# Optimization experiments

Measured on AMD Instinct MI355X. Metric: run time of the kernel, lower is better.

Reference implementation:

```python
import jax, jax.numpy as jnp
import numpy as np

EPS = 1.01e-08
BN_EPS = 1e-5

def conv2d(x, w, b, stride, padding):
    y = jax.lax.conv_general_dilated(x, w, window_strides=stride, padding=padding,
                                     dimension_numbers=('NCHW', 'OIHW', 'NCHW'))
    return y + b[None, :, None, None]

def masknorm(x, mask, mask_norm):
    amp = jnp.sqrt(jnp.sum(x * x, axis=1, keepdims=True) + EPS)  # (B,1,F,T)
    if mask is None:
        return x / amp
    if mask_norm:
        mask_sum = jnp.sum(mask, axis=(2, 3), keepdims=True)
        return x * mask / (amp * mask_sum)
    return x * mask / amp

def flow_attention(q, k, v):
    # Flowformer linear attention, single head. q,k,v: (B, L, D)
    q = jax.nn.sigmoid(q)
    k = jax.nn.sigmoid(k)
    L = q.shape[1]
    sink_in = 1.0 / (jnp.einsum('bld,bd->bl', q + EPS, k.sum(1) + EPS))
    src_out = 1.0 / (jnp.einsum('bld,bd->bl', k + EPS, q.sum(1) + EPS))
    cons_sink = jnp.einsum('bld,bd->bl', q + EPS, (k * src_out[..., None]).sum(1) + EPS)
    cons_src = jnp.einsum('bld,bd->bl', k + EPS, (q * sink_in[..., None]).sum(1) + EPS)
    sink_alloc = jax.nn.sigmoid(cons_sink)
    src_comp = jax.nn.softmax(cons_src, axis=-1) * jnp.asarray(L, q.dtype)
    kv = jnp.einsum('bld,blm->bdm', k, v * src_comp[..., None])  # (B,D,D)
    out = jnp.einsum('bld,bdm->blm', q, kv) * sink_in[..., None] * sink_alloc[..., None]
    return out

def setup_inputs() -> dict:
    key = jax.random.key(0)
    ks = jax.random.split(key, 16)
    B, Cin, H, T = 4, 8, 252, 2048
    D = 12  # emb_dims
    inp = {
        'x': jax.random.normal(ks[0], (B, Cin, H, T), jnp.float32),
        'frame': jax.random.uniform(ks[1], (B, 1, 84, T), jnp.float32),
        # CBLR: Conv2d(8,16,5x5,same) + BatchNorm2d(16) + LeakyReLU
        'w_pre': jax.random.normal(ks[2], (16, 8, 5, 5), jnp.float32) * 0.05,
        'b_pre': jnp.zeros((16,), jnp.float32),
        'bn_gamma': jnp.ones((16,), jnp.float32),
        'bn_beta': jnp.zeros((16,), jnp.float32),
        'bn_mean': jnp.zeros((16,), jnp.float32),
        'bn_var': jnp.ones((16,), jnp.float32),
        'T': jnp.asarray(2.0, jnp.float32),
        'wq_conv': jax.random.normal(ks[3], (D, 16, 3, 3), jnp.float32) * 0.05,
        'bq_conv': jnp.zeros((D,), jnp.float32),
        'wkv_conv': jax.random.normal(ks[4], (D, 16, 3, 3), jnp.float32) * 0.05,
        'bkv_conv': jnp.zeros((D,), jnp.float32),
        # FlowAttention projections (single head, d_model = emb_dims = 12)
        'fa_wq': jax.random.normal(ks[5], (D, D), jnp.float32) * 0.3,
        'fa_bq': jnp.zeros((D,), jnp.float32),
        'fa_wk': jax.random.normal(ks[6], (D, D), jnp.float32) * 0.3,
        'fa_bk': jnp.zeros((D,), jnp.float32),
        'fa_wv': jax.random.normal(ks[7], (D, D), jnp.float32) * 0.3,
        'fa_bv': jnp.zeros((D,), jnp.float32),
        'fa_wo': jax.random.normal(ks[8], (D, D), jnp.float32) * 0.3,
        'fa_bo': jnp.zeros((D,), jnp.float32),
    }
    return inp

def reference(x, frame, w_pre, b_pre, bn_gamma, bn_beta, bn_mean, bn_var, T,
              wq_conv, bq_conv, wkv_conv, bkv_conv,
              fa_wq, fa_bq, fa_wk, fa_bk, fa_wv, fa_bv, fa_wo, fa_bo):
    # pre_encoding: Conv(same) -> BatchNorm(eval) -> LeakyReLU(0.01)
    h = conv2d(x, w_pre, b_pre, (1, 1), [(2, 2), (2, 2)])
    h = (h - bn_mean[None, :, None, None]) * jax.lax.rsqrt(bn_var + BN_EPS)[None, :, None, None]
    h = h * bn_gamma[None, :, None, None] + bn_beta[None, :, None, None]
    h = jnp.where(h >= 0, h, 0.01 * h)
    # embedding convs: kernel 3x3, stride (3,1), padding (0,1) -> (B,D,84,T)
    KV = conv2d(h, wkv_conv, bkv_conv, (3, 1), [(0, 0), (1, 1)])
    KV = masknorm(KV, frame, True) * T
    Q = conv2d(h, wq_conv, bq_conv, (3, 1), [(0, 0), (1, 1)])
    B, D, Fb, Tt = Q.shape
    # flatten spatial grid to a sequence of length L = F*T
    q = Q.reshape(B, D, Fb * Tt).transpose(0, 2, 1)
    kv = KV.reshape(B, D, Fb * Tt).transpose(0, 2, 1)
    qp = q @ fa_wq + fa_bq
    kp = kv @ fa_wk + fa_bk
    vp = kv @ fa_wv + fa_bv
    o = flow_attention(qp, kp, vp)
    o = o @ fa_wo + fa_bo  # dropout disabled (eval)
    emb = o.transpose(0, 2, 1).reshape(B, D, Fb, Tt)
    return emb
```

## Files before the change

### kernel.cpp

```cpp
#include <hip/hip_runtime.h>
#include <math.h>

#define EPSF 1.01e-08f

namespace {
constexpr int NB = 4;
constexpr int HH = 252, TW = 2048;
constexpr int C1 = 16, DD = 12, FF = 84;
constexpr int LLEN = FF * TW;

constexpr size_t OFF_H   = 0;
constexpr size_t SZ_H    = (size_t)NB * C1 * HH * TW;
constexpr size_t SZ_QKV  = (size_t)NB * LLEN * DD;
constexpr size_t OFF_Q   = OFF_H + SZ_H;
constexpr size_t OFF_K   = OFF_Q + SZ_QKV;
constexpr size_t OFF_V   = OFF_K + SZ_QKV;
constexpr size_t OFF_SI  = OFF_V + SZ_QKV;
constexpr size_t OFF_SA  = OFF_SI + (size_t)NB * LLEN;
constexpr size_t OFF_WP  = OFF_SA + (size_t)NB * LLEN;
constexpr size_t OFF_B1  = OFF_WP + 3200;
constexpr size_t OFF_WQT = OFF_B1 + 16;
constexpr size_t OFF_WKT = OFF_WQT + 1728;
constexpr size_t FTOT    = OFF_WKT + 1728;
constexpr size_t DBYTE   = FTOT * sizeof(float);

constexpr int DO_MSUM = 0;
constexpr int DO_KSUM = 4;
constexpr int DO_QSUM = 52;
constexpr int DO_SKQ  = 100;
constexpr int DO_SQS  = 148;
constexpr int DO_SE   = 196;
constexpr int DO_M    = 200;
constexpr int NDBL    = 776;
}

__device__ __forceinline__ float wsum(float v) {
#pragma unroll
  for (int m = 1; m < 64; m <<= 1) v += __shfl_xor(v, m, 64);
  return v;
}
__device__ __forceinline__ double wsumd(double v) {
#pragma unroll
  for (int m = 1; m < 64; m <<= 1) v += __shfl_xor(v, m, 64);
  return v;
}
__device__ __forceinline__ void atomAddD(double* p, double v) { unsafeAtomicAdd(p, v); }
__device__ __forceinline__ float sigm(float x) { return 1.f / (1.f + expf(-x)); }

__global__ void k_prep(const float* __restrict__ w_pre, const float* __restrict__ b_pre,
                       const float* __restrict__ g, const float* __restrict__ be,
                       const float* __restrict__ mean, const float* __restrict__ var,
                       const float* __restrict__ wq, const float* __restrict__ wkv,
                       float* __restrict__ ws) {
  int tid = blockIdx.x * 256 + threadIdx.x;
  int stride = gridDim.x * 256;
  if (tid < 16) {
    float sc = g[tid] / sqrtf(var[tid] + 1e-5f);
    ws[OFF_B1 + tid] = (b_pre[tid] - mean[tid]) * sc + be[tid];
  }
  for (int idx = tid; idx < 3200; idx += stride) {
    int co = idx & 15, r = idx >> 4;
    int ci = r / 25, p = r % 25;
    float sc = g[co] / sqrtf(var[co] + 1e-5f);
    ws[OFF_WP + idx] = w_pre[(co * 8 + ci) * 25 + p] * sc;
  }
  for (int idx = tid; idx < 1728; idx += stride) {
    int d = idx % 12, r = idx / 12;
    ws[OFF_WQT + idx] = wq[d * 144 + r];
    ws[OFF_WKT + idx] = wkv[d * 144 + r];
  }
}

__global__ __launch_bounds__(256, 4) void k_conv1(const float* __restrict__ x,
                                                  const float* __restrict__ wsc,
                                                  float* __restrict__ h) {
  __shared__ __align__(16) float xs[6][520];

  const int cb = blockIdx.x * 512;
  const int y0 = blockIdx.y * 2;
  const int b = blockIdx.z;

  float acc[16][2][2];
#pragma unroll
  for (int co = 0; co < 16; co++)
#pragma unroll
    for (int r = 0; r < 2; r++)
#pragma unroll
      for (int c = 0; c < 2; c++) acc[co][r][c] = 0.f;

  const int lc = (int)threadIdx.x * 2;

  for (int ci = 0; ci < 8; ci++) {
    __syncthreads();
    const float* xc = x + (size_t)(b * 8 + ci) * HH * TW;
    for (int li = threadIdx.x; li < 6 * 520; li += 256) {
      const int r = li / 520;
      const int c = li - r * 520;
      const int gy = y0 - 2 + r;
      const int gx = cb - 2 + c;
      float v = 0.f;
      if (gy >= 0 && gy < HH && gx >= 0 && gx < TW) v = xc[(size_t)gy * TW + gx];
      xs[r][c] = v;
    }
    __syncthreads();

#pragma unroll
    for (int kh = 0; kh < 5; kh++) {
      float ra[6], rb[6];
#pragma unroll
      for (int u = 0; u < 3; u++) {
        const float2 a = *(const float2*)(&xs[kh][lc + 2 * u]);
        const float2 bv = *(const float2*)(&xs[kh + 1][lc + 2 * u]);
        ra[2 * u] = a.x; ra[2 * u + 1] = a.y;
        rb[2 * u] = bv.x; rb[2 * u + 1] = bv.y;
      }
      const float* wrow = wsc + OFF_WP + (size_t)(ci * 25 + kh * 5) * 16;
#pragma unroll
      for (int kw = 0; kw < 5; kw++) {
        const float4 wA = *(const float4*)(wrow + kw * 16);
        const float4 wB = *(const float4*)(wrow + kw * 16 + 4);
        const float4 wC = *(const float4*)(wrow + kw * 16 + 8);
        const float4 wD = *(const float4*)(wrow + kw * 16 + 12);
        const float wv[16] = {wA.x, wA.y, wA.z, wA.w, wB.x, wB.y, wB.z, wB.w,
                              wC.x, wC.y, wC.z, wC.w, wD.x, wD.y, wD.z, wD.w};
        const float x00 = ra[kw], x01 = ra[kw + 1];
        const float x10 = rb[kw], x11 = rb[kw + 1];
#pragma unroll
        for (int co = 0; co < 16; co++) {
          acc[co][0][0] = fmaf(x00, wv[co], acc[co][0][0]);
          acc[co][0][1] = fmaf(x01, wv[co], acc[co][0][1]);
          acc[co][1][0] = fmaf(x10, wv[co], acc[co][1][0]);
          acc[co][1][1] = fmaf(x11, wv[co], acc[co][1][1]);
        }
      }
    }
  }

#pragma unroll
  for (int co = 0; co < 16; co++) {
    const float bb = wsc[OFF_B1 + co];
#pragma unroll
    for (int r = 0; r < 2; r++) {
      float2 o;
      const float z0 = acc[co][r][0] + bb; o.x = (z0 >= 0.f) ? z0 : 0.01f * z0;
      const float z1 = acc[co][r][1] + bb; o.y = (z1 >= 0.f) ? z1 : 0.01f * z1;
      *(float2*)(h + ((size_t)(b * 16 + co) * HH + (y0 + r)) * TW + cb + lc) = o;
    }
  }
}

__global__ void k_masksum(const float* __restrict__ frame, double* __restrict__ dacc) {
  const int b = blockIdx.y;
  const float* fr = frame + (size_t)b * FF * TW;
  double s = 0.0;
  for (int i = blockIdx.x * 256 + threadIdx.x; i < FF * TW; i += gridDim.x * 256)
    s += (double)fr[i];
  s = wsumd(s);
  __shared__ double sm[4];
  int lane = threadIdx.x & 63, wid = threadIdx.x >> 6;
  if (lane == 0) sm[wid] = s;
  __syncthreads();
  if (threadIdx.x == 0) atomAddD(&dacc[DO_MSUM + b], sm[0] + sm[1] + sm[2] + sm[3]);
}

__global__ __launch_bounds__(256, 3) void k_conv2q(
    const float* __restrict__ h, const float* __restrict__ wsc,
    double* __restrict__ dacc,
    const float* __restrict__ fwq, const float* __restrict__ fbq,
    const float* __restrict__ bqc,
    float* __restrict__ qo) {
  const int c0 = (blockIdx.x * 256 + threadIdx.x) * 4;
  const int f = blockIdx.y;
  const int b = blockIdx.z;
  const bool interior = (c0 >= 4) && (c0 + 8 <= TW);

  float aq[12][4];
#pragma unroll
  for (int d = 0; d < 12; d++) {
    const float bq = bqc[d];
#pragma unroll
    for (int j = 0; j < 4; j++) aq[d][j] = bq;
  }

  for (int c = 0; c < 16; c++) {
    const float* hc = h + ((size_t)(b * 16 + c) * HH + 3 * f) * TW;
#pragma unroll
    for (int kh = 0; kh < 3; kh++) {
      const float* row = hc + (size_t)kh * TW;
      float xr[12];
      if (interior) {
#pragma unroll
        for (int v = 0; v < 3; v++)
          *(float4*)(xr + 4 * v) = *(const float4*)(row + c0 - 4 + 4 * v);
      } else {
#pragma unroll
        for (int j = 0; j < 12; j++) {
          int cc = c0 - 4 + j;
          xr[j] = (cc >= 0 && cc < TW) ? row[cc] : 0.f;
        }
      }
      const float* wp = wsc + OFF_WQT + (size_t)(c * 9 + kh * 3) * 12;
#pragma unroll
      for (int kw = 0; kw < 3; kw++) {
        const float4 w0 = *(const float4*)(wp + kw * 12);
        const float4 w1 = *(const float4*)(wp + kw * 12 + 4);
        const float4 w2 = *(const float4*)(wp + kw * 12 + 8);
        const float wv[12] = {w0.x, w0.y, w0.z, w0.w, w1.x, w1.y, w1.z, w1.w,
                              w2.x, w2.y, w2.z, w2.w};
#pragma unroll
        for (int j = 0; j < 4; j++) {
          const float xv = xr[3 + kw + j];
#pragma unroll
          for (int d = 0; d < 12; d++) aq[d][j] = fmaf(xv, wv[d], aq[d][j]);
        }
      }
    }
  }

  float s1[12][4];
#pragma unroll
  for (int d = 0; d < 12; d++) {
    const float bb = fbq[d];
#pragma unroll
    for (int j = 0; j < 4; j++) s1[d][j] = bb;
  }
#pragma unroll
  for (int e = 0; e < 12; e++) {
    const float4 w0 = *(const float4*)(fwq + e * 12);
    const float4 w1 = *(const float4*)(fwq + e * 12 + 4);
    const float4 w2 = *(const float4*)(fwq + e * 12 + 8);
    const float wv[12] = {w0.x, w0.y, w0.z, w0.w, w1.x, w1.y, w1.z, w1.w,
                          w2.x, w2.y, w2.z, w2.w};
#pragma unroll
    for (int j = 0; j < 4; j++) {
      const float a = aq[e][j];
#pragma unroll
      for (int d = 0; d < 12; d++) s1[d][j] = fmaf(a, wv[d], s1[d][j]);
    }
  }

  float qsumP[12];
#pragma unroll
  for (int d = 0; d < 12; d++) qsumP[d] = 0.f;
  const size_t lbase = (size_t)f * TW + c0;
#pragma unroll
  for (int j = 0; j < 4; j++) {
    const size_t o = ((size_t)b * LLEN + lbase + j) * 12;
#pragma unroll
    for (int d = 0; d < 12; d++) {
      const float qv = sigm(s1[d][j]);
      qsumP[d] += qv;
      qo[o + d] = qv;
    }
  }

  __shared__ float red[4 * 12];
  int lane = threadIdx.x & 63, wid = threadIdx.x >> 6;
#pragma unroll
  for (int d = 0; d < 12; d++) {
    float s = wsum(qsumP[d]);
    if (lane == 0) red[wid * 12 + d] = s;
  }
  __syncthreads();
  if (threadIdx.x < 12) {
    float tot = red[threadIdx.x] + red[12 + threadIdx.x] + red[24 + threadIdx.x] + red[36 + threadIdx.x];
    atomAddD(&dacc[DO_QSUM + b * 12 + threadIdx.x], (double)tot);
  }
}

__global__ __launch_bounds__(256, 3) void k_conv2kv(
    const float* __restrict__ h, const float* __restrict__ frame,
    const float* __restrict__ wsc, double* __restrict__ dacc,
    const float* __restrict__ fwk, const float* __restrict__ fbk,
    const float* __restrict__ fwv, const float* __restrict__ fbv,
    const float* __restrict__ bkvc, const float* __restrict__ Tp,
    float* __restrict__ ko, float* __restrict__ vo) {
  const int c0 = (blockIdx.x * 256 + threadIdx.x) * 4;
  const int f = blockIdx.y;
  const int b = blockIdx.z;
  const bool interior = (c0 >= 4) && (c0 + 8 <= TW);

  float akv[12][4];
#pragma unroll
  for (int d = 0; d < 12; d++) {
    const float bk = bkvc[d];
#pragma unroll
    for (int j = 0; j < 4; j++) akv[d][j] = bk;
  }

  for (int c = 0; c < 16; c++) {
    const float* hc = h + ((size_t)(b * 16 + c) * HH + 3 * f) * TW;
#pragma unroll
    for (int kh = 0; kh < 3; kh++) {
      const float* row = hc + (size_t)kh * TW;
      float xr[12];
      if (interior) {
#pragma unroll
        for (int v = 0; v < 3; v++)
          *(float4*)(xr + 4 * v) = *(const float4*)(row + c0 - 4 + 4 * v);
      } else {
#pragma unroll
        for (int j = 0; j < 12; j++) {
          int cc = c0 - 4 + j;
          xr[j] = (cc >= 0 && cc < TW) ? row[cc] : 0.f;
        }
      }
      const float* wp = wsc + OFF_WKT + (size_t)(c * 9 + kh * 3) * 12;
#pragma unroll
      for (int kw = 0; kw < 3; kw++) {
        const float4 w0 = *(const float4*)(wp + kw * 12);
        const float4 w1 = *(const float4*)(wp + kw * 12 + 4);
        const float4 w2 = *(const float4*)(wp + kw * 12 + 8);
        const float wv[12] = {w0.x, w0.y, w0.z, w0.w, w1.x, w1.y, w1.z, w1.w,
                              w2.x, w2.y, w2.z, w2.w};
#pragma unroll
        for (int j = 0; j < 4; j++) {
          const float xv = xr[3 + kw + j];
#pragma unroll
          for (int d = 0; d < 12; d++) akv[d][j] = fmaf(xv, wv[d], akv[d][j]);
        }
      }
    }
  }

  const float msum = (float)dacc[DO_MSUM + b];
  const float Tv = Tp[0];
  const float4 mk4 = *(const float4*)(frame + ((size_t)b * FF + f) * TW + c0);
  const float mks[4] = {mk4.x, mk4.y, mk4.z, mk4.w};
#pragma unroll
  for (int j = 0; j < 4; j++) {
    float ss = EPSF;
#pragma unroll
    for (int d = 0; d < 12; d++) ss = fmaf(akv[d][j], akv[d][j], ss);
    const float sc = mks[j] * Tv / (sqrtf(ss) * msum);
#pragma unroll
    for (int d = 0; d < 12; d++) akv[d][j] *= sc;
  }

  const size_t lbase = (size_t)f * TW + c0;
  float ksumP[12];
#pragma unroll
  for (int d = 0; d < 12; d++) ksumP[d] = 0.f;

  {
    float s2[12][4];
#pragma unroll
    for (int d = 0; d < 12; d++) {
      const float bb = fbk[d];
#pragma unroll
      for (int j = 0; j < 4; j++) s2[d][j] = bb;
    }
#pragma unroll
    for (int e = 0; e < 12; e++) {
      const float4 w0 = *(const float4*)(fwk + e * 12);
      const float4 w1 = *(const float4*)(fwk + e * 12 + 4);
      const float4 w2 = *(const float4*)(fwk + e * 12 + 8);
      const float wv[12] = {w0.x, w0.y, w0.z, w0.w, w1.x, w1.y, w1.z, w1.w,
                            w2.x, w2.y, w2.z, w2.w};
#pragma unroll
      for (int j = 0; j < 4; j++) {
        const float a = akv[e][j];
#pragma unroll
        for (int d = 0; d < 12; d++) s2[d][j] = fmaf(a, wv[d], s2[d][j]);
      }
    }
#pragma unroll
    for (int j = 0; j < 4; j++) {
      const size_t o = ((size_t)b * LLEN + lbase + j) * 12;
#pragma unroll
      for (int d = 0; d < 12; d++) {
        const float kk = sigm(s2[d][j]);
        ksumP[d] += kk;
        ko[o + d] = kk;
      }
    }
  }

  {
    float s3[12][4];
#pragma unroll
    for (int d = 0; d < 12; d++) {
      const float bb = fbv[d];
#pragma unroll
      for (int j = 0; j < 4; j++) s3[d][j] = bb;
    }
#pragma unroll
    for (int e = 0; e < 12; e++) {
      const float4 w0 = *(const float4*)(fwv + e * 12);
      const float4 w1 = *(const float4*)(fwv + e * 12 + 4);
      const float4 w2 = *(const float4*)(fwv + e * 12 + 8);
      const float wv[12] = {w0.x, w0.y, w0.z, w0.w, w1.x, w1.y, w1.z, w1.w,
                            w2.x, w2.y, w2.z, w2.w};
#pragma unroll
      for (int j = 0; j < 4; j++) {
        const float a = akv[e][j];
#pragma unroll
        for (int d = 0; d < 12; d++) s3[d][j] = fmaf(a, wv[d], s3[d][j]);
      }
    }
#pragma unroll
    for (int j = 0; j < 4; j++) {
      const size_t o = ((size_t)b * LLEN + lbase + j) * 12;
#pragma unroll
      for (int d = 0; d < 12; d++) vo[o + d] = s3[d][j];
    }
  }

  __shared__ float red[4 * 12];
  int lane = threadIdx.x & 63, wid = threadIdx.x >> 6;
#pragma unroll
  for (int d = 0; d < 12; d++) {
    float s = wsum(ksumP[d]);
    if (lane == 0) red[wid * 12 + d] = s;
  }
  __syncthreads();
  if (threadIdx.x < 12) {
    float tot = red[threadIdx.x] + red[12 + threadIdx.x] + red[24 + threadIdx.x] + red[36 + threadIdx.x];
    atomAddD(&dacc[DO_KSUM + b * 12 + threadIdx.x], (double)tot);
  }
}

__global__ __launch_bounds__(256) void k_sink(const float* __restrict__ q,
                                              const float* __restrict__ k,
                                              float* __restrict__ sink_in,
                                              double* __restrict__ dacc) {
  const int b = blockIdx.y;
  const int tid0 = blockIdx.x * 256 + threadIdx.x;
  float ksE[12], qsE[12];
#pragma unroll
  for (int d = 0; d < 12; d++) {
    ksE[d] = (float)(dacc[DO_KSUM + b * 12 + d] + (double)EPSF);
    qsE[d] = (float)(dacc[DO_QSUM + b * 12 + d] + (double)EPSF);
  }
  float askq[12], asqs[12];
#pragma unroll
  for (int d = 0; d < 12; d++) { askq[d] = 0.f; asqs[d] = 0.f; }
  for (int it = 0; it < 8; it++) {
    size_t l = (size_t)it * 21504 + tid0;
    const float* qp = q + ((size_t)b * LLEN + l) * 12;
    const float* kp = k + ((size_t)b * LLEN + l) * 12;
    float qv[12], kv[12];
#pragma unroll
    for (int d = 0; d < 12; d++) { qv[d] = qp[d]; kv[d] = kp[d]; }
    float s1 = 0.f, s2 = 0.f;
#pragma unroll
    for (int d = 0; d < 12; d++) {
      s1 = fmaf(qv[d] + EPSF, ksE[d], s1);
      s2 = fmaf(kv[d] + EPSF, qsE[d], s2);
    }
    float si = 1.f / s1;
    float so = 1.f / s2;
    sink_in[(size_t)b * LLEN + l] = si;
#pragma unroll
    for (int d = 0; d < 12; d++) {
      askq[d] = fmaf(kv[d], so, askq[d]);
      asqs[d] = fmaf(qv[d], si, asqs[d]);
    }
  }
  float part[24];
#pragma unroll
  for (int d = 0; d < 12; d++) { part[d] = askq[d]; part[12 + d] = asqs[d]; }
  __shared__ float red[4 * 24];
  int lane = threadIdx.x & 63, wid = threadIdx.x >> 6;
#pragma unroll
  for (int j = 0; j < 24; j++) {
    float s = wsum(part[j]);
    if (lane == 0) red[wid * 24 + j] = s;
  }
  __syncthreads();
  if (threadIdx.x < 24) {
    float tot = red[threadIdx.x] + red[24 + threadIdx.x] + red[48 + threadIdx.x] + red[72 + threadIdx.x];
    int idx = (threadIdx.x < 12) ? (DO_SKQ + b * 12 + threadIdx.x)
                                 : (DO_SQS + b * 12 + (threadIdx.x - 12));
    atomAddD(&dacc[idx], (double)tot);
  }
}

__global__ __launch_bounds__(256) void k_flow(const float* __restrict__ q,
                                              const float* __restrict__ k,
                                              const float* __restrict__ v,
                                              float* __restrict__ sink_alloc,
                                              double* __restrict__ dacc) {
  const int b = blockIdx.y;
  const int tid0 = blockIdx.x * 256 + threadIdx.x;
  float skqE[12], sqsE[12];
#pragma unroll
  for (int d = 0; d < 12; d++) {
    skqE[d] = (float)(dacc[DO_SKQ + b * 12 + d] + (double)EPSF);
    sqsE[d] = (float)(dacc[DO_SQS + b * 12 + d] + (double)EPSF);
  }
  float acc[144];
#pragma unroll
  for (int j = 0; j < 144; j++) acc[j] = 0.f;
  double se = 0.0;
  for (int it = 0; it < 4; it++) {
    size_t l = (size_t)it * 43008 + tid0;
    size_t o = ((size_t)b * LLEN + l) * 12;
    float qv[12], kv[12], vv[12];
#pragma unroll
    for (int d = 0; d < 12; d++) { qv[d] = q[o + d]; kv[d] = k[o + d]; vv[d] = v[o + d]; }
    float c1 = 0.f, c2 = 0.f;
#pragma unroll
    for (int d = 0; d < 12; d++) {
      c1 = fmaf(qv[d] + EPSF, skqE[d], c1);
      c2 = fmaf(kv[d] + EPSF, sqsE[d], c2);
    }
    sink_alloc[(size_t)b * LLEN + l] = sigm(c1);
    float e = expf(c2);
    se += (double)e;
#pragma unroll
    for (int d = 0; d < 12; d++) {
      float ke = kv[d] * e;
#pragma unroll
      for (int m = 0; m < 12; m++) acc[d * 12 + m] = fmaf(ke, vv[m], acc[d * 12 + m]);
    }
  }
  __shared__ float red[4 * 144];
  __shared__ double seds[4];
  int lane = threadIdx.x & 63, wid = threadIdx.x >> 6;
#pragma unroll
  for (int j = 0; j < 144; j++) {
    float s = wsum(acc[j]);
    if (lane == 0) red[wid * 144 + j] = s;
  }
  double sew = wsumd(se);
  if (lane == 0) seds[wid] = sew;
  __syncthreads();
  if (threadIdx.x < 144) {
    float tot = red[threadIdx.x] + red[144 + threadIdx.x] + red[288 + threadIdx.x] + red[432 + threadIdx.x];
    atomAddD(&dacc[DO_M + b * 144 + threadIdx.x], (double)tot);
  }
  if (threadIdx.x == 192) atomAddD(&dacc[DO_SE + b], seds[0] + seds[1] + seds[2] + seds[3]);
}

__global__ __launch_bounds__(256) void k_out(const float* __restrict__ q,
                                             const float* __restrict__ sink_in,
                                             const float* __restrict__ sink_alloc,
                                             const double* __restrict__ dacc,
                                             const float* __restrict__ wo,
                                             const float* __restrict__ bo,
                                             float* __restrict__ out) {
  const int t = blockIdx.x * 256 + threadIdx.x;
  const int f = blockIdx.y;
  const int b = blockIdx.z;
  __shared__ float kvf[144];
  if (threadIdx.x < 144) {
    double fac = (double)LLEN / dacc[DO_SE + b];
    kvf[threadIdx.x] = (float)(dacc[DO_M + b * 144 + threadIdx.x] * fac);
  }
  __syncthreads();
  size_t l = (size_t)f * TW + t;
  const float* qp = q + ((size_t)b * LLEN + l) * 12;
  float qv[12];
#pragma unroll
  for (int d = 0; d < 12; d++) qv[d] = qp[d];
  float s = sink_in[(size_t)b * LLEN + l] * sink_alloc[(size_t)b * LLEN + l];
  float o[12];
#pragma unroll
  for (int m = 0; m < 12; m++) {
    float a = 0.f;
#pragma unroll
    for (int d = 0; d < 12; d++) a = fmaf(qv[d], kvf[d * 12 + m], a);
    o[m] = a * s;
  }
#pragma unroll
  for (int m2 = 0; m2 < 12; m2++) {
    float a = bo[m2];
#pragma unroll
    for (int m = 0; m < 12; m++) a = fmaf(o[m], wo[m * 12 + m2], a);
    out[((size_t)b * 12 + m2) * LLEN + l] = a;
  }
}

extern "C" void kernel_launch(void* const* d_in, const int* in_sizes, int n_in,
                              void* d_out, int out_size, void* d_ws, size_t ws_size,
                              hipStream_t stream) {
  (void)in_sizes; (void)n_in; (void)out_size; (void)ws_size;
  const float* x     = (const float*)d_in[0];
  const float* frame = (const float*)d_in[1];
  const float* w_pre = (const float*)d_in[2];
  const float* b_pre = (const float*)d_in[3];
  const float* gam   = (const float*)d_in[4];
  const float* bet   = (const float*)d_in[5];
  const float* mean  = (const float*)d_in[6];
  const float* var   = (const float*)d_in[7];
  const float* Tp    = (const float*)d_in[8];
  const float* wq_c  = (const float*)d_in[9];
  const float* bq_c  = (const float*)d_in[10];
  const float* wkv_c = (const float*)d_in[11];
  const float* bkv_c = (const float*)d_in[12];
  const float* fa_wq = (const float*)d_in[13];
  const float* fa_bq = (const float*)d_in[14];
  const float* fa_wk = (const float*)d_in[15];
  const float* fa_bk = (const float*)d_in[16];
  const float* fa_wv = (const float*)d_in[17];
  const float* fa_bv = (const float*)d_in[18];
  const float* fa_wo = (const float*)d_in[19];
  const float* fa_bo = (const float*)d_in[20];

  float* ws = (float*)d_ws;
  double* dacc = (double*)((char*)d_ws + DBYTE);
  float* out = (float*)d_out;

  hipMemsetAsync(dacc, 0, NDBL * sizeof(double), stream);
  k_prep<<<dim3(16), 256, 0, stream>>>(w_pre, b_pre, gam, bet, mean, var, wq_c, wkv_c, ws);
  k_masksum<<<dim3(64, 4), 256, 0, stream>>>(frame, dacc);
  k_conv1<<<dim3(4, 126, 4), 256, 0, stream>>>(x, ws, ws + OFF_H);
  k_conv2q<<<dim3(2, 84, 4), 256, 0, stream>>>(ws + OFF_H, ws, dacc,
      fa_wq, fa_bq, bq_c, ws + OFF_Q);
  k_conv2kv<<<dim3(2, 84, 4), 256, 0, stream>>>(ws + OFF_H, frame, ws, dacc,
      fa_wk, fa_bk, fa_wv, fa_bv, bkv_c, Tp, ws + OFF_K, ws + OFF_V);
  k_sink<<<dim3(84, 4), 256, 0, stream>>>(ws + OFF_Q, ws + OFF_K, ws + OFF_SI, dacc);
  k_flow<<<dim3(168, 4), 256, 0, stream>>>(ws + OFF_Q, ws + OFF_K, ws + OFF_V, ws + OFF_SA, dacc);
  k_out<<<dim3(8, 84, 4), 256, 0, stream>>>(ws + OFF_Q, ws + OFF_SI, ws + OFF_SA, dacc,
      fa_wo, fa_bo, out);
}
```

Baseline: 694.2 us.

## Retile pre-conv so each wavefront owns 4 output channels over 8 columns

Restructures the 5x5 conv kernel so each wavefront computes 4 output channels over 2 rows by 8 columns per thread, instead of every thread computing all 16 channels for 2x2 pixels. Weights are staged in LDS rather than read through scalar/global loads. The input tile is stored with an XOR swizzle on float4 groups to avoid LDS bank conflicts on the wider vector reads. This aims to raise register reuse of input values and cut LDS read traffic per FMA. In exchange it adds LDS usage, lowers the occupancy hint to 3 blocks, and has each wavefront redundantly read the shared input row.

```diff
diff --git a/kernel.cpp b/kernel.cpp
--- a/kernel.cpp
+++ b/kernel.cpp
@@ -71,80 +71,93 @@
   }
 }
 
-__global__ __launch_bounds__(256, 4) void k_conv1(const float* __restrict__ x,
+__global__ __launch_bounds__(256, 3) void k_conv1(const float* __restrict__ x,
                                                   const float* __restrict__ wsc,
                                                   float* __restrict__ h) {
-  __shared__ __align__(16) float xs[6][520];
+  __shared__ __align__(16) float wl[3200];
+  __shared__ float bl[16];
+  __shared__ __align__(16) float xs[6][544];
 
   const int cb = blockIdx.x * 512;
   const int y0 = blockIdx.y * 2;
   const int b = blockIdx.z;
-
-  float acc[16][2][2];
-#pragma unroll
-  for (int co = 0; co < 16; co++)
+  const int g = threadIdx.x >> 6;
+  const int lane = threadIdx.x & 63;
+  const int c0 = cb + lane * 8;
+
+  for (int i = threadIdx.x * 4; i < 3200; i += 1024)
+    *(float4*)(wl + i) = *(const float4*)(wsc + OFF_WP + i);
+  if (threadIdx.x < 16) bl[threadIdx.x] = wsc[OFF_B1 + threadIdx.x];
+
+  float acc[4][2][8];
+#pragma unroll
+  for (int co = 0; co < 4; co++)
 #pragma unroll
     for (int r = 0; r < 2; r++)
 #pragma unroll
-      for (int c = 0; c < 2; c++) acc[co][r][c] = 0.f;
-
-  const int lc = (int)threadIdx.x * 2;
+      for (int j = 0; j < 8; j++) acc[co][r][j] = 0.f;
 
   for (int ci = 0; ci < 8; ci++) {
     __syncthreads();
     const float* xc = x + (size_t)(b * 8 + ci) * HH * TW;
-    for (int li = threadIdx.x; li < 6 * 520; li += 256) {
-      const int r = li / 520;
-      const int c = li - r * 520;
+    for (int li = threadIdx.x; li < 6 * 528; li += 256) {
+      const int r = li / 528;
+      const int c = li - r * 528;
       const int gy = y0 - 2 + r;
-      const int gx = cb - 2 + c;
+      const int gx = cb - 4 + c;
       float v = 0.f;
       if (gy >= 0 && gy < HH && gx >= 0 && gx < TW) v = xc[(size_t)gy * TW + gx];
-      xs[r][c] = v;
+      const int q = c >> 2;
+      const int sq = q ^ ((q >> 3) & 7);
+      xs[r][sq * 4 + (c & 3)] = v;
     }
     __syncthreads();
 
 #pragma unroll
     for (int kh = 0; kh < 5; kh++) {
-      float ra[6], rb[6];
-#pragma unroll
-      for (int u = 0; u < 3; u++) {
-        const float2 a = *(const float2*)(&xs[kh][lc + 2 * u]);
-        const float2 bv = *(const float2*)(&xs[kh + 1][lc + 2 * u]);
-        ra[2 * u] = a.x; ra[2 * u + 1] = a.y;
-        rb[2 * u] = bv.x; rb[2 * u + 1] = bv.y;
-      }
-      const float* wrow = wsc + OFF_WP + (size_t)(ci * 25 + kh * 5) * 16;
+      float ra[16], rb[16];
+#pragma unroll
+      for (int k = 0; k < 4; k++) {
+        const int q = lane * 2 + k;
+        const int sq = q ^ ((q >> 3) & 7);
+        *(float4*)(ra + 4 * k) = *(const float4*)(&xs[kh][sq * 4]);
+        *(float4*)(rb + 4 * k) = *(const float4*)(&xs[kh + 1][sq * 4]);
+      }
+      const float* wrow = wl + (ci * 25 + kh * 5) * 16 + g * 4;
 #pragma unroll
       for (int kw = 0; kw < 5; kw++) {
-        const float4 wA = *(const float4*)(wrow + kw * 16);
-        const float4 wB = *(const float4*)(wrow + kw * 16 + 4);
-        const float4 wC = *(const float4*)(wrow + kw * 16 + 8);
-        const float4 wD = *(const float4*)(wrow + kw * 16 + 12);
-        const float wv[16] = {wA.x, wA.y, wA.z, wA.w, wB.x, wB.y, wB.z, wB.w,
-                              wC.x, wC.y, wC.z, wC.w, wD.x, wD.y, wD.z, wD.w};
-        const float x00 = ra[kw], x01 = ra[kw + 1];
-        const float x10 = rb[kw], x11 = rb[kw + 1];
-#pragma unroll
-        for (int co = 0; co < 16; co++) {
-          acc[co][0][0] = fmaf(x00, wv[co], acc[co][0][0]);
-          acc[co][0][1] = fmaf(x01, wv[co], acc[co][0][1]);
-          acc[co][1][0] = fmaf(x10, wv[co], acc[co][1][0]);
-          acc[co][1][1] = fmaf(x11, wv[co], acc[co][1][1]);
-        }
-      }
-    }
-  }
-
-#pragma unroll
-  for (int co = 0; co < 16; co++) {
-    const float bb = wsc[OFF_B1 + co];
+        const float4 w4 = *(const float4*)(wrow + kw * 16);
+        const float wv[4] = {w4.x, w4.y, w4.z, w4.w};
+#pragma unroll
+        for (int co = 0; co < 4; co++)
+#pragma unroll
+          for (int j = 0; j < 8; j++) {
+            acc[co][0][j] = fmaf(ra[2 + kw + j], wv[co], acc[co][0][j]);
+            acc[co][1][j] = fmaf(rb[2 + kw + j], wv[co], acc[co][1][j]);
+          }
+      }
+    }
+  }
+
+#pragma unroll
+  for (int co = 0; co < 4; co++) {
+    const float bb = bl[g * 4 + co];
+    const size_t rowbase = (size_t)(b * 16 + g * 4 + co) * HH;
 #pragma unroll
     for (int r = 0; r < 2; r++) {
-      float2 o;
-      const float z0 = acc[co][r][0] + bb; o.x = (z0 >= 0.f) ? z0 : 0.01f * z0;
-      const float z1 = acc[co][r][1] + bb; o.y = (z1 >= 0.f) ? z1 : 0.01f * z1;
-      *(float2*)(h + ((size_t)(b * 16 + co) * HH + (y0 + r)) * TW + cb + lc) = o;
+      float4 o0, o1;
+      float z;
+      z = acc[co][r][0] + bb; o0.x = (z >= 0.f) ? z : 0.01f * z;
+      z = acc[co][r][1] + bb; o0.y = (z >= 0.f) ? z : 0.01f * z;
+      z = acc[co][r][2] + bb; o0.z = (z >= 0.f) ? z : 0.01f * z;
+      z = acc[co][r][3] + bb; o0.w = (z >= 0.f) ? z : 0.01f * z;
+      z = acc[co][r][4] + bb; o1.x = (z >= 0.f) ? z : 0.01f * z;
+      z = acc[co][r][5] + bb; o1.y = (z >= 0.f) ? z : 0.01f * z;
+      z = acc[co][r][6] + bb; o1.z = (z >= 0.f) ? z : 0.01f * z;
+      z = acc[co][r][7] + bb; o1.w = (z >= 0.f) ? z : 0.01f * z;
+      float* hp = h + (rowbase + (y0 + r)) * TW + c0;
+      *(float4*)(hp) = o0;
+      *(float4*)(hp + 4) = o1;
     }
   }
 }
```

After: 646.4 us. 6.9% less time.
